# Optimization experiments

Hardware: AMD Instinct MI355X
Metric: run time of the kernel (lower is better)

## Reference

```python
import jax, jax.numpy as jnp
import numpy as np
from jax import lax

N, H, W, CIN = 64, 256, 256, 3   # batch, image HxW, RGB
C, K = 32, 5                     # cross-conv channels / kernel size (from reshape(-1,32,5,5))
ADIM, AHID = 4, 256              # action dim, action-encoder hidden


def _conv(x, w, b, stride, pad):
    # x [N,C,H,W], w [O,I,kh,kw] (torch OIHW cross-correlation semantics)
    y = lax.conv_general_dilated(x, w, (stride, stride), [(pad, pad), (pad, pad)],
                                 dimension_numbers=('NCHW', 'OIHW', 'NCHW'))
    return y + b[None, :, None, None]


def cross_convolve(feat, kernels):
    # feat [N,C,h,w], kernels [N,C,K,K]; per-sample per-channel 'same' conv (padding=2).
    # Equivalent to the original N*C loop of tiny F.conv2d calls: one depthwise
    # (grouped, feature_group_count=C) conv per sample, vmapped over the batch.
    def one(x, k):  # x [C,h,w], k [C,K,K]
        y = lax.conv_general_dilated(x[None], k[:, None], (1, 1), [(2, 2), (2, 2)],
                                     dimension_numbers=('NCHW', 'OIHW', 'NCHW'),
                                     feature_group_count=C)
        return y[0]
    return jax.vmap(one)(feat, kernels)


def setup_inputs() -> dict:
    key = jax.random.key(0)
    ks = jax.random.split(key, 10)
    g = lambda i, shape, s: jax.random.normal(ks[i], shape, jnp.float32) * s
    return {
        'images': jax.random.normal(ks[0], (N, H, W, CIN), jnp.float32),
        'actions': jax.random.normal(ks[1], (N, ADIM), jnp.float32),
        # phys_encoder: conv(3->32,k5,s2,p2) relu, conv(32->32,k5,s2,p2) relu
        'pe_w1': g(2, (C, CIN, 5, 5), 0.08), 'pe_b1': jnp.zeros((C,), jnp.float32),
        'pe_w2': g(3, (C, C, 5, 5), 0.04), 'pe_b2': jnp.zeros((C,), jnp.float32),
        # action_encoder MLP: ADIM -> AHID -> C*K*K (=800)
        'ae_w1': g(4, (ADIM, AHID), 0.3), 'ae_b1': jnp.zeros((AHID,), jnp.float32),
        'ae_w2': g(5, (AHID, C * K * K), 0.05), 'ae_b2': jnp.zeros((C * K * K,), jnp.float32),
        # motion_predictor: conv(32->32,k3,p1) relu, conv(32->2,k3,p1)
        'mp_w1': g(6, (C, C, 3, 3), 0.06), 'mp_b1': jnp.zeros((C,), jnp.float32),
        'mp_w2': g(7, (2, C, 3, 3), 0.06), 'mp_b2': jnp.zeros((2,), jnp.float32),
    }


def reference(images, actions, pe_w1, pe_b1, pe_w2, pe_b2,
              ae_w1, ae_b1, ae_w2, ae_b2, mp_w1, mp_b1, mp_w2, mp_b2):
    x = jnp.transpose(images, (0, 3, 1, 2))                 # NHWC -> NCHW
    h = jax.nn.relu(_conv(x, pe_w1, pe_b1, 2, 2))           # [N,32,128,128]
    h = jax.nn.relu(_conv(h, pe_w2, pe_b2, 2, 2))           # [N,32,64,64]
    a = jax.nn.relu(actions @ ae_w1 + ae_b1)
    a = (a @ ae_w2 + ae_b2).reshape(-1, C, K, K)            # per-sample kernels [N,32,5,5]
    sa = cross_convolve(h, a)                               # [N,32,64,64]
    f = jax.nn.relu(_conv(sa, mp_w1, mp_b1, 1, 1))
    flow = _conv(f, mp_w2, mp_b2, 1, 1)                     # [N,2,64,64]
    return flow
```

## Files before the change

### kernel.cpp

```cpp
#include <hip/hip_runtime.h>


typedef __attribute__((ext_vector_type(8))) short bf16x8;
typedef __attribute__((ext_vector_type(4))) float f32x4;
typedef __attribute__((ext_vector_type(16))) float f32x16;

__device__ __forceinline__ unsigned short f2bf(float f) {
    unsigned int u = __float_as_uint(f);
    u = (u + 0x7FFFu + ((u >> 16) & 1u)) >> 16;
    return (unsigned short)u;
}
__device__ __forceinline__ float bf2f(unsigned short h) {
    return __uint_as_float(((unsigned int)h) << 16);
}

__global__ __launch_bounds__(64) void zero_border2(unsigned int* t0, int R0, int p0,
                                                   unsigned int* t1, int R1, int p1) {
    unsigned int* t = blockIdx.y ? t1 : t0;
    const int R = blockIdx.y ? R1 : R0;
    const int pad = blockIdx.y ? p1 : p0;
    const int row = blockIdx.x % R;
    const int n = blockIdx.x / R;
    if (n >= 64) return;
    const int tid = threadIdx.x;
    unsigned int* rp = t + (size_t)(n * R + row) * R * 16;
    if (row < pad || row >= R - pad) {
        for (int i = tid; i < R * 16; i += 64) rp[i] = 0u;
    } else {
        for (int i = tid; i < pad * 16; i += 64) {
            rp[i] = 0u;
            rp[(size_t)(R - pad) * 16 + i] = 0u;
        }
    }
}

__global__ __launch_bounds__(64) void zero_border_eo(unsigned int* E, unsigned int* O) {
    unsigned int* t = blockIdx.y ? O : E;
    const int row = blockIdx.x % 132;
    const int n = blockIdx.x / 132;
    const int tid = threadIdx.x;
    unsigned int* rp = t + (size_t)(n * 132 + row) * (66 * 16);
    if (row < 2 || row >= 130) {
        for (int i = tid; i < 66 * 16; i += 64) rp[i] = 0u;
    } else if (tid < 16) {
        rp[tid] = 0u;
        rp[65 * 16 + tid] = 0u;
    }
}

__global__ __launch_bounds__(256) void pad_img_kernel(const float* __restrict__ img,
                                                      unsigned short* __restrict__ imgp) {
    const int py = blockIdx.x % 260;
    const int n  = blockIdx.x / 260;
    const int iy = py - 2;
    const bool rowok = (iy >= 0) && (iy < 256);
    const float* srow = img + ((size_t)n * 256 + (rowok ? iy : 0)) * 768;
    unsigned short* drow = imgp + (size_t)(n * 260 + py) * 1056;
    for (int s = threadIdx.x; s < 1056; s += 256) {
        int px = s >> 2, c = s & 3;
        int ix = px - 2;
        float v = 0.f;
        if (rowok && c < 3 && ix >= 0 && ix < 256) v = srow[ix * 3 + c];
        drow[s] = f2bf(v);
    }
}

__global__ __launch_bounds__(256) void repack_all(const float* __restrict__ pe_w1,
                                                  const float* __restrict__ pe_w2,
                                                  const float* __restrict__ mp_w1,
                                                  const float* __restrict__ mp_w2,
                                                  unsigned short* __restrict__ B1,
                                                  unsigned short* __restrict__ B2,
                                                  unsigned short* __restrict__ Bm1,
                                                  unsigned short* __restrict__ Bm2) {
    int idx = blockIdx.x * 256 + threadIdx.x;
    if (idx < 5120) {
        int kh = idx / 1024, r = idx % 1024, o = r / 32, k = r % 32, dx = k >> 2, c = k & 3;
        float v = (dx < 5 && c < 3) ? pe_w1[o * 75 + c * 25 + kh * 5 + dx] : 0.f;
        B1[idx] = f2bf(v);
    } else if (idx < 30720) {
        int i = idx - 5120;
        int co = i / 800, r = i % 800, ci = r / 25, tap = r % 25;
        B2[(tap * 32 + co) * 32 + ci] = f2bf(pe_w2[i]);
    } else if (idx < 39936) {
        int i = idx - 30720;
        int co = i / 288, r = i % 288, ci = r / 9, tap = r % 9;
        Bm1[(tap * 32 + co) * 32 + ci] = f2bf(mp_w1[i]);
    } else if (idx < 44544) {
        int i = idx - 39936;
        int tap = i / 512, r = i % 512, co = r / 32, ci = r % 32;
        float v = (co < 2) ? mp_w2[co * 288 + ci * 9 + tap] : 0.f;
        Bm2[i] = f2bf(v);
    }
}

__global__ __launch_bounds__(256) void mlp_kernel(const float* __restrict__ actions,
                                                  const float* __restrict__ w1,
                                                  const float* __restrict__ b1,
                                                  const float* __restrict__ w2,
                                                  const float* __restrict__ b2,
                                                  float* __restrict__ aout) {
    int n = blockIdx.y;
    int t = threadIdx.x;
    __shared__ float hid[256];
    float a0 = actions[n * 4 + 0], a1 = actions[n * 4 + 1];
    float a2 = actions[n * 4 + 2], a3 = actions[n * 4 + 3];
    float acc = b1[t];
    acc += a0 * w1[0 * 256 + t] + a1 * w1[1 * 256 + t] +
           a2 * w1[2 * 256 + t] + a3 * w1[3 * 256 + t];
    hid[t] = fmaxf(acc, 0.0f);
    __syncthreads();
    int o = blockIdx.x * 200 + t;
    if (t < 200) {
        float s = b2[o];
        #pragma unroll 4
        for (int i = 0; i < 256; ++i) s += hid[i] * w2[i * 800 + o];
        aout[n * 800 + o] = s;
    }
}

__global__ __launch_bounds__(256, 4) void conv1_mfma(const unsigned short* __restrict__ imgp,
                                                     const short* __restrict__ B1,
                                                     const float* __restrict__ bias,
                                                     unsigned short* __restrict__ h1e,
                                                     unsigned short* __restrict__ h1o) {
    const int tid = threadIdx.x;
    const int lane = tid & 63;
    const int w = tid >> 6;
    const int n = blockIdx.y;
    const int cohalf = w & 1;
    const int oy = blockIdx.x * 2 + (w >> 1);
    const int ml = lane & 15;
    const int kg = lane >> 4;

    bf16x8 bfrag[5];
    #pragma unroll
    for (int kh = 0; kh < 5; ++kh)
        bfrag[kh] = *(const bf16x8*)(B1 + ((kh * 32 + cohalf * 16 + ml) * 32 + kg * 8));
    const float bia = bias[cohalf * 16 + ml];
    const int co = cohalf * 16 + ml;

    f32x4 acc[8];
    #pragma unroll
    for (int t = 0; t < 8; ++t) acc[t] = (f32x4){bia, bia, bia, bia};

    #pragma unroll
    for (int kh = 0; kh < 5; ++kh) {
        const unsigned short* rowbase = imgp + (size_t)(n * 260 + 2 * oy + kh) * 1056;
        bf16x8 af[8];
        #pragma unroll
        for (int t = 0; t < 8; ++t) {
            const int px0 = 2 * (16 * t + ml) + 2 * kg;
            af[t] = *(const bf16x8*)(rowbase + px0 * 4);
        }
        __builtin_amdgcn_sched_barrier(0);
        #pragma unroll
        for (int t = 0; t < 8; ++t)
            acc[t] = __builtin_amdgcn_mfma_f32_16x16x32_bf16(af[t], bfrag[kh], acc[t], 0, 0, 0);
    }
    const size_t rowoff = ((size_t)(n * 132) + oy + 2) * 2112 + co;
    #pragma unroll
    for (int t = 0; t < 8; ++t) {
        #pragma unroll
        for (int r = 0; r < 4; ++r) {
            const int px = 16 * t + kg * 4 + r;
            const unsigned short v = f2bf(fmaxf(acc[t][r], 0.f));
            if ((r & 1) == 0) h1e[rowoff + (size_t)((px + 2) >> 1) * 32] = v;
            else              h1o[rowoff + (size_t)((px + 1) >> 1) * 32] = v;
        }
    }
}

__global__ __launch_bounds__(256, 4) void conv2_mfma32(const unsigned short* __restrict__ h1e,
                                                       const unsigned short* __restrict__ h1o,
                                                       const unsigned int* __restrict__ B,
                                                       const float* __restrict__ bias,
                                                       unsigned short* __restrict__ h2p) {
    __shared__ unsigned int Bs[5 * 32 * 20];
    const int tid = threadIdx.x;
    const int lane = tid & 63;
    const int w = tid >> 6;
    const int n = blockIdx.y;
    const int oy = blockIdx.x * 2 + (w >> 1);
    const int x0 = (w & 1) * 32;
    const int ml = lane & 31;
    const int kgrp = lane >> 5;

    const float bia = bias[ml];
    f32x16 accA, accB;
    #pragma unroll
    for (int r = 0; r < 16; ++r) { accA[r] = bia; accB[r] = 0.f; }

    const unsigned short* bbase = (const unsigned short*)Bs + ml * 40 + kgrp * 8;
    const int qbase = (x0 + ml) * 32 + kgrp * 8;

    for (int kh = 0; kh < 5; ++kh) {
        if (kh) __syncthreads();
        const unsigned int* src = B + kh * 2560;
        #pragma unroll
        for (int i = tid; i < 2560; i += 256) {
            int row = i >> 4, p = i & 15;
            Bs[row * 20 + p] = src[i];
        }
        __syncthreads();

        const size_t rowoff = ((size_t)(n * 132) + 2 * oy + kh) * 2112;
        const unsigned short* re = h1e + rowoff + qbase;
        const unsigned short* ro = h1o + rowoff + qbase;
        bf16x8 ae[6], ao[4];
        #pragma unroll
        for (int j = 0; j < 3; ++j) {
            ae[2 * j]     = *(const bf16x8*)(re + j * 32);
            ae[2 * j + 1] = *(const bf16x8*)(re + j * 32 + 16);
        }
        #pragma unroll
        for (int j = 0; j < 2; ++j) {
            ao[2 * j]     = *(const bf16x8*)(ro + j * 32);
            ao[2 * j + 1] = *(const bf16x8*)(ro + j * 32 + 16);
        }
        __builtin_amdgcn_sched_barrier(0);
        #pragma unroll
        for (int j = 0; j < 3; ++j) {
            const bf16x8 b0 = *(const bf16x8*)(bbase + (2 * j) * 1280);
            const bf16x8 b1 = *(const bf16x8*)(bbase + (2 * j) * 1280 + 16);
            accA = __builtin_amdgcn_mfma_f32_32x32x16_bf16(ae[2 * j], b0, accA, 0, 0, 0);
            accA = __builtin_amdgcn_mfma_f32_32x32x16_bf16(ae[2 * j + 1], b1, accA, 0, 0, 0);
        }
        #pragma unroll
        for (int j = 0; j < 2; ++j) {
            const bf16x8 b0 = *(const bf16x8*)(bbase + (2 * j + 1) * 1280);
            const bf16x8 b1 = *(const bf16x8*)(bbase + (2 * j + 1) * 1280 + 16);
            accB = __builtin_amdgcn_mfma_f32_32x32x16_bf16(ao[2 * j], b0, accB, 0, 0, 0);
            accB = __builtin_amdgcn_mfma_f32_32x32x16_bf16(ao[2 * j + 1], b1, accB, 0, 0, 0);
        }
    }
    #pragma unroll
    for (int r = 0; r < 16; ++r) {
        const int px = (r & 3) + 8 * (r >> 2) + 4 * kgrp;
        const int ox = x0 + px;
        h2p[((size_t)(n * 68 + oy + 2) * 68 + ox + 2) * 32 + ml] =
            f2bf(fmaxf(accA[r] + accB[r], 0.f));
    }
}

__global__ __launch_bounds__(256) void xconv_kernel(const unsigned short* __restrict__ h2p,
                                                    const float* __restrict__ ker,
                                                    unsigned short* __restrict__ sap) {
    __shared__ __align__(16) unsigned short tile[12 * 68 * 32];
    const int tid = threadIdx.x;
    const int n = blockIdx.x;
    const int rb = blockIdx.y;
    const unsigned short* src = h2p + (size_t)(n * 68 + rb * 8) * (68 * 32);
    for (int i = tid; i < 3264; i += 256)
        *(uint4*)(tile + i * 8) = *(const uint4*)(src + i * 8);
    const int ci = tid & 31, xg = tid >> 5;
    const float* kp = ker + (size_t)(n * 32 + ci) * 25;
    float k[25];
    #pragma unroll
    for (int t = 0; t < 25; ++t) k[t] = kp[t];
    __syncthreads();

    float acc[8][8];
    #pragma unroll
    for (int r = 0; r < 8; ++r)
        #pragma unroll
        for (int j = 0; j < 8; ++j) acc[r][j] = 0.f;

    #pragma unroll
    for (int ir = 0; ir < 12; ++ir) {
        float v[12];
        #pragma unroll
        for (int t = 0; t < 12; ++t)
            v[t] = bf2f(tile[(ir * 68 + xg * 8 + t) * 32 + ci]);
        #pragma unroll
        for (int kh = 0; kh < 5; ++kh) {
            const int r = ir - kh;
            if (r >= 0 && r < 8) {
                #pragma unroll
                for (int j = 0; j < 8; ++j) {
                    float s = acc[r][j];
                    #pragma unroll
                    for (int kw = 0; kw < 5; ++kw) s += k[kh * 5 + kw] * v[j + kw];
                    acc[r][j] = s;
                }
            }
        }
    }
    #pragma unroll
    for (int r = 0; r < 8; ++r)
        #pragma unroll
        for (int j = 0; j < 8; ++j)
            sap[((size_t)(n * 66 + rb * 8 + r + 1) * 66 + xg * 8 + j + 1) * 32 + ci] = f2bf(acc[r][j]);
}

__global__ __launch_bounds__(256, 4) void mp1_mfma32(const unsigned short* __restrict__ sap,
                                                     const unsigned int* __restrict__ B,
                                                     const float* __restrict__ bias,
                                                     unsigned short* __restrict__ fp) {
    __shared__ unsigned int Bs[9 * 32 * 20];
    const int tid = threadIdx.x;
    #pragma unroll
    for (int i = tid; i < 4608; i += 256) {
        int row = i >> 4, p = i & 15;
        Bs[row * 20 + p] = B[i];
    }
    __syncthreads();

    const int lane = tid & 63;
    const int w = tid >> 6;
    const int n = blockIdx.y;
    const int oy = blockIdx.x * 2 + (w >> 1);
    const int x0 = (w & 1) * 32;
    const int ml = lane & 31;
    const int kgrp = lane >> 5;

    const float bia = bias[ml];
    f32x16 accA, accB;
    #pragma unroll
    for (int r = 0; r < 16; ++r) { accA[r] = bia; accB[r] = 0.f; }

    const unsigned short* bbase = (const unsigned short*)Bs + ml * 40 + kgrp * 8;
    const int px0 = x0 + ml;

    #pragma unroll
    for (int kh = 0; kh < 3; ++kh) {
        const unsigned short* rowbase = sap + (size_t)(n * 66 + oy + kh) * 2112 + kgrp * 8;
        bf16x8 a[6];
        #pragma unroll
        for (int kw = 0; kw < 3; ++kw) {
            a[2 * kw]     = *(const bf16x8*)(rowbase + (px0 + kw) * 32);
            a[2 * kw + 1] = *(const bf16x8*)(rowbase + (px0 + kw) * 32 + 16);
        }
        __builtin_amdgcn_sched_barrier(0);
        #pragma unroll
        for (int kw = 0; kw < 3; ++kw) {
            const int tap = kh * 3 + kw;
            const bf16x8 b0 = *(const bf16x8*)(bbase + tap * 1280);
            const bf16x8 b1 = *(const bf16x8*)(bbase + tap * 1280 + 16);
            if (tap & 1) {
                accB = __builtin_amdgcn_mfma_f32_32x32x16_bf16(a[2 * kw], b0, accB, 0, 0, 0);
                accB = __builtin_amdgcn_mfma_f32_32x32x16_bf16(a[2 * kw + 1], b1, accB, 0, 0, 0);
            } else {
                accA = __builtin_amdgcn_mfma_f32_32x32x16_bf16(a[2 * kw], b0, accA, 0, 0, 0);
                accA = __builtin_amdgcn_mfma_f32_32x32x16_bf16(a[2 * kw + 1], b1, accA, 0, 0, 0);
            }
        }
    }
    #pragma unroll
    for (int r = 0; r < 16; ++r) {
        const int px = (r & 3) + 8 * (r >> 2) + 4 * kgrp;
        const int ox = x0 + px;
        fp[((size_t)(n * 66 + oy + 1) * 66 + ox + 1) * 32 + ml] =
            f2bf(fmaxf(accA[r] + accB[r], 0.f));
    }
}

__global__ __launch_bounds__(256, 4) void mp2_mfma(const unsigned short* __restrict__ fpb,
                                                   const short* __restrict__ B,
                                                   const float* __restrict__ bias,
                                                   float* __restrict__ out) {
    const int tid = threadIdx.x;
    const int lane = tid & 63;
    const int w = tid >> 6;
    const int n = blockIdx.y;
    const int oy = blockIdx.x * 4 + w;
    const int ml = lane & 15;
    const int kg = lane >> 4;

    bf16x8 bfrag[9];
    #pragma unroll
    for (int t = 0; t < 9; ++t)
        bfrag[t] = *(const bf16x8*)(B + ((t * 16 + ml) * 32 + kg * 8));
    const float bia = (ml < 2) ? bias[ml] : 0.f;

    f32x4 acc[4];
    #pragma unroll
    for (int t = 0; t < 4; ++t) acc[t] = (f32x4){bia, bia, bia, bia};

    #pragma unroll
    for (int kh = 0; kh < 3; ++kh) {
        const unsigned short* rowbase = fpb + (size_t)(n * 66 + oy + kh) * (66 * 32);
        bf16x8 af[12];
        #pragma unroll
        for (int kw = 0; kw < 3; ++kw)
            #pragma unroll
            for (int t = 0; t < 4; ++t)
                af[kw * 4 + t] = *(const bf16x8*)(rowbase + (16 * t + ml + kw) * 32 + kg * 8);
        __builtin_amdgcn_sched_barrier(0);
        #pragma unroll
        for (int kw = 0; kw < 3; ++kw)
            #pragma unroll
            for (int t = 0; t < 4; ++t)
                acc[t] = __builtin_amdgcn_mfma_f32_16x16x32_bf16(af[kw * 4 + t], bfrag[kh * 3 + kw], acc[t], 0, 0, 0);
    }
    if (ml < 2) {
        #pragma unroll
        for (int t = 0; t < 4; ++t) {
            #pragma unroll
            for (int r = 0; r < 4; ++r) {
                const int px = 16 * t + kg * 4 + r;
                out[(size_t)n * 8192 + (size_t)ml * 4096 + (size_t)oy * 64 + px] = acc[t][r];
            }
        }
    }
}

extern "C" void kernel_launch(void* const* d_in, const int* in_sizes, int n_in,
                              void* d_out, int out_size, void* d_ws, size_t ws_size,
                              hipStream_t stream) {
    (void)in_sizes; (void)n_in; (void)out_size; (void)ws_size;
    const float* images  = (const float*)d_in[0];
    const float* actions = (const float*)d_in[1];
    const float* pe_w1   = (const float*)d_in[2];
    const float* pe_b1   = (const float*)d_in[3];
    const float* pe_w2   = (const float*)d_in[4];
    const float* pe_b2   = (const float*)d_in[5];
    const float* ae_w1   = (const float*)d_in[6];
    const float* ae_b1   = (const float*)d_in[7];
    const float* ae_w2   = (const float*)d_in[8];
    const float* ae_b2   = (const float*)d_in[9];
    const float* mp_w1   = (const float*)d_in[10];
    const float* mp_b1   = (const float*)d_in[11];
    const float* mp_w2   = (const float*)d_in[12];
    const float* mp_b2   = (const float*)d_in[13];
    float* out = (float*)d_out;

    char* ws = (char*)d_ws;
    float* a_ker          = (float*)(ws + 0);
    unsigned short* B1    = (unsigned short*)(ws + 204800);
    unsigned short* B2    = (unsigned short*)(ws + 215040);
    unsigned short* Bm1   = (unsigned short*)(ws + 266240);
    unsigned short* Bm2   = (unsigned short*)(ws + 284672);
    unsigned short* h1e   = (unsigned short*)(ws + 524288);
    unsigned short* h1o   = (unsigned short*)(ws + 36208640);
    unsigned short* imgp  = (unsigned short*)(ws + 71892992);
    unsigned short* h2p   = (unsigned short*)(ws + 71892992);
    unsigned short* sap   = (unsigned short*)(ws + 90832896);
    unsigned short* fpb   = (unsigned short*)(ws + 108675072);

    repack_all<<<174, 256, 0, stream>>>(pe_w1, pe_w2, mp_w1, mp_w2, B1, B2, Bm1, Bm2);
    mlp_kernel<<<dim3(4, 64), 256, 0, stream>>>(actions, ae_w1, ae_b1, ae_w2, ae_b2, a_ker);
    zero_border_eo<<<dim3(64 * 132, 2), 64, 0, stream>>>((unsigned int*)h1e, (unsigned int*)h1o);
    zero_border2<<<dim3(64 * 66, 1), 64, 0, stream>>>((unsigned int*)fpb, 66, 1,
                                                      (unsigned int*)fpb, 66, 1);

    pad_img_kernel<<<64 * 260, 256, 0, stream>>>(images, imgp);
    conv1_mfma<<<dim3(64, 64), 256, 0, stream>>>(imgp, (const short*)B1, pe_b1, h1e, h1o);

    zero_border2<<<dim3(64 * 68, 2), 64, 0, stream>>>((unsigned int*)h2p, 68, 2,
                                                      (unsigned int*)sap, 66, 1);

    conv2_mfma32<<<dim3(32, 64), 256, 0, stream>>>(h1e, h1o, (const unsigned int*)B2, pe_b2, h2p);
    xconv_kernel<<<dim3(64, 8), 256, 0, stream>>>(h2p, a_ker, sap);
    mp1_mfma32<<<dim3(32, 64), 256, 0, stream>>>(sap, (const unsigned int*)Bm1, mp_b1, fpb);
    mp2_mfma<<<dim3(16, 64), 256, 0, stream>>>(fpb, (const short*)Bm2, mp_b2, out);
}
```

Baseline: 279.5 us.

## Swap MFMA operands to vectorize channel-contiguous epilogue stores across conv kernels

Conv1, conv2 and mp1 now pass the weight fragment as the MFMA A operand, so each lane's accumulator rows cover consecutive output channels. That lets the epilogues pack four bf16 values into a single 8-byte store instead of issuing scattered 2-byte stores. Bias is added at the end from a vector load rather than used to seed the accumulators. The cross-conv kernel stages its output through shared memory so it can write 16-byte coalesced rows, and the image pad kernel now writes one packed 8-byte pixel per thread. In exchange this adds extra shared-memory traffic and syncs in the cross-conv kernel.

```diff
diff --git a/kernel.cpp b/kernel.cpp
--- a/kernel.cpp
+++ b/kernel.cpp
@@ -9,6 +9,9 @@
     unsigned int u = __float_as_uint(f);
     u = (u + 0x7FFFu + ((u >> 16) & 1u)) >> 16;
     return (unsigned short)u;
+}
+__device__ __forceinline__ unsigned int pk2(float lo, float hi) {
+    return (unsigned int)f2bf(lo) | ((unsigned int)f2bf(hi) << 16);
 }
 __device__ __forceinline__ float bf2f(unsigned short h) {
     return __uint_as_float(((unsigned int)h) << 16);
@@ -56,12 +59,14 @@
     const bool rowok = (iy >= 0) && (iy < 256);
     const float* srow = img + ((size_t)n * 256 + (rowok ? iy : 0)) * 768;
     unsigned short* drow = imgp + (size_t)(n * 260 + py) * 1056;
-    for (int s = threadIdx.x; s < 1056; s += 256) {
-        int px = s >> 2, c = s & 3;
-        int ix = px - 2;
-        float v = 0.f;
-        if (rowok && c < 3 && ix >= 0 && ix < 256) v = srow[ix * 3 + c];
-        drow[s] = f2bf(v);
+    for (int px = threadIdx.x; px < 264; px += 256) {
+        const int ix = px - 2;
+        float c0 = 0.f, c1 = 0.f, c2 = 0.f;
+        if (rowok && ix >= 0 && ix < 256) {
+            c0 = srow[ix * 3 + 0]; c1 = srow[ix * 3 + 1]; c2 = srow[ix * 3 + 2];
+        }
+        uint2 u; u.x = pk2(c0, c1); u.y = pk2(c2, 0.f);
+        *(uint2*)(drow + px * 4) = u;
     }
 }
 
@@ -137,12 +142,10 @@
     #pragma unroll
     for (int kh = 0; kh < 5; ++kh)
         bfrag[kh] = *(const bf16x8*)(B1 + ((kh * 32 + cohalf * 16 + ml) * 32 + kg * 8));
-    const float bia = bias[cohalf * 16 + ml];
-    const int co = cohalf * 16 + ml;
 
     f32x4 acc[8];
     #pragma unroll
-    for (int t = 0; t < 8; ++t) acc[t] = (f32x4){bia, bia, bia, bia};
+    for (int t = 0; t < 8; ++t) acc[t] = (f32x4){0.f, 0.f, 0.f, 0.f};
 
     #pragma unroll
     for (int kh = 0; kh < 5; ++kh) {
@@ -156,18 +159,19 @@
         __builtin_amdgcn_sched_barrier(0);
         #pragma unroll
         for (int t = 0; t < 8; ++t)
-            acc[t] = __builtin_amdgcn_mfma_f32_16x16x32_bf16(af[t], bfrag[kh], acc[t], 0, 0, 0);
-    }
-    const size_t rowoff = ((size_t)(n * 132) + oy + 2) * 2112 + co;
+            acc[t] = __builtin_amdgcn_mfma_f32_16x16x32_bf16(bfrag[kh], af[t], acc[t], 0, 0, 0);
+    }
+    const f32x4 b4 = *(const f32x4*)(bias + cohalf * 16 + kg * 4);
+    const int cobase = cohalf * 16 + kg * 4;
+    const size_t rowoff = ((size_t)(n * 132) + oy + 2) * 2112;
     #pragma unroll
     for (int t = 0; t < 8; ++t) {
-        #pragma unroll
-        for (int r = 0; r < 4; ++r) {
-            const int px = 16 * t + kg * 4 + r;
-            const unsigned short v = f2bf(fmaxf(acc[t][r], 0.f));
-            if ((r & 1) == 0) h1e[rowoff + (size_t)((px + 2) >> 1) * 32] = v;
-            else              h1o[rowoff + (size_t)((px + 1) >> 1) * 32] = v;
-        }
+        const int px = 16 * t + ml;
+        uint2 uv;
+        uv.x = pk2(fmaxf(acc[t][0] + b4[0], 0.f), fmaxf(acc[t][1] + b4[1], 0.f));
+        uv.y = pk2(fmaxf(acc[t][2] + b4[2], 0.f), fmaxf(acc[t][3] + b4[3], 0.f));
+        if (ml & 1) *(uint2*)(h1o + rowoff + (size_t)((px + 1) >> 1) * 32 + cobase) = uv;
+        else        *(uint2*)(h1e + rowoff + (size_t)((px + 2) >> 1) * 32 + cobase) = uv;
     }
 }
 
@@ -186,10 +190,9 @@
     const int ml = lane & 31;
     const int kgrp = lane >> 5;
 
-    const float bia = bias[ml];
     f32x16 accA, accB;
     #pragma unroll
-    for (int r = 0; r < 16; ++r) { accA[r] = bia; accB[r] = 0.f; }
+    for (int r = 0; r < 16; ++r) { accA[r] = 0.f; accB[r] = 0.f; }
 
     const unsigned short* bbase = (const unsigned short*)Bs + ml * 40 + kgrp * 8;
     const int qbase = (x0 + ml) * 32 + kgrp * 8;
@@ -223,23 +226,30 @@
         for (int j = 0; j < 3; ++j) {
             const bf16x8 b0 = *(const bf16x8*)(bbase + (2 * j) * 1280);
             const bf16x8 b1 = *(const bf16x8*)(bbase + (2 * j) * 1280 + 16);
-            accA = __builtin_amdgcn_mfma_f32_32x32x16_bf16(ae[2 * j], b0, accA, 0, 0, 0);
-            accA = __builtin_amdgcn_mfma_f32_32x32x16_bf16(ae[2 * j + 1], b1, accA, 0, 0, 0);
+            accA = __builtin_amdgcn_mfma_f32_32x32x16_bf16(b0, ae[2 * j], accA, 0, 0, 0);
+            accA = __builtin_amdgcn_mfma_f32_32x32x16_bf16(b1, ae[2 * j + 1], accA, 0, 0, 0);
         }
         #pragma unroll
         for (int j = 0; j < 2; ++j) {
             const bf16x8 b0 = *(const bf16x8*)(bbase + (2 * j + 1) * 1280);
             const bf16x8 b1 = *(const bf16x8*)(bbase + (2 * j + 1) * 1280 + 16);
-            accB = __builtin_amdgcn_mfma_f32_32x32x16_bf16(ao[2 * j], b0, accB, 0, 0, 0);
-            accB = __builtin_amdgcn_mfma_f32_32x32x16_bf16(ao[2 * j + 1], b1, accB, 0, 0, 0);
-        }
-    }
-    #pragma unroll
-    for (int r = 0; r < 16; ++r) {
-        const int px = (r & 3) + 8 * (r >> 2) + 4 * kgrp;
-        const int ox = x0 + px;
-        h2p[((size_t)(n * 68 + oy + 2) * 68 + ox + 2) * 32 + ml] =
-            f2bf(fmaxf(accA[r] + accB[r], 0.f));
+            accB = __builtin_amdgcn_mfma_f32_32x32x16_bf16(b0, ao[2 * j], accB, 0, 0, 0);
+            accB = __builtin_amdgcn_mfma_f32_32x32x16_bf16(b1, ao[2 * j + 1], accB, 0, 0, 0);
+        }
+    }
+    const int px = x0 + ml;
+    unsigned short* dst = h2p + ((size_t)(n * 68 + oy + 2) * 68 + px + 2) * 32;
+    #pragma unroll
+    for (int g = 0; g < 4; ++g) {
+        const f32x4 b4 = *(const f32x4*)(bias + 8 * g + 4 * kgrp);
+        float a0 = accA[4 * g + 0] + accB[4 * g + 0] + b4[0];
+        float a1 = accA[4 * g + 1] + accB[4 * g + 1] + b4[1];
+        float a2 = accA[4 * g + 2] + accB[4 * g + 2] + b4[2];
+        float a3 = accA[4 * g + 3] + accB[4 * g + 3] + b4[3];
+        uint2 uv;
+        uv.x = pk2(fmaxf(a0, 0.f), fmaxf(a1, 0.f));
+        uv.y = pk2(fmaxf(a2, 0.f), fmaxf(a3, 0.f));
+        *(uint2*)(dst + 8 * g + 4 * kgrp) = uv;
     }
 }
 
@@ -286,11 +296,18 @@
             }
         }
     }
+    __syncthreads();
     #pragma unroll
     for (int r = 0; r < 8; ++r)
         #pragma unroll
         for (int j = 0; j < 8; ++j)
-            sap[((size_t)(n * 66 + rb * 8 + r + 1) * 66 + xg * 8 + j + 1) * 32 + ci] = f2bf(acc[r][j]);
+            tile[(r * 64 + xg * 8 + j) * 32 + ci] = f2bf(acc[r][j]);
+    __syncthreads();
+    #pragma unroll
+    for (int r = 0; r < 8; ++r) {
+        uint4 v = *(const uint4*)(tile + (size_t)r * 2048 + tid * 8);
+        *(uint4*)(sap + ((size_t)(n * 66 + rb * 8 + r + 1) * 66 + 1) * 32 + tid * 8) = v;
+    }
 }
 
 __global__ __launch_bounds__(256, 4) void mp1_mfma32(const unsigned short* __restrict__ sap,
@@ -314,10 +331,9 @@
     const int ml = lane & 31;
     const int kgrp = lane >> 5;
 
-    const float bia = bias[ml];
     f32x16 accA, accB;
     #pragma unroll
-    for (int r = 0; r < 16; ++r) { accA[r] = bia; accB[r] = 0.f; }
+    for (int r = 0; r < 16; ++r) { accA[r] = 0.f; accB[r] = 0.f; }
 
     const unsigned short* bbase = (const unsigned short*)Bs + ml * 40 + kgrp * 8;
     const int px0 = x0 + ml;
@@ -338,20 +354,27 @@
             const bf16x8 b0 = *(const bf16x8*)(bbase + tap * 1280);
             const bf16x8 b1 = *(const bf16x8*)(bbase + tap * 1280 + 16);
             if (tap & 1) {
-                accB = __builtin_amdgcn_mfma_f32_32x32x16_bf16(a[2 * kw], b0, accB, 0, 0, 0);
-                accB = __builtin_amdgcn_mfma_f32_32x32x16_bf16(a[2 * kw + 1], b1, accB, 0, 0, 0);
+                accB = __builtin_amdgcn_mfma_f32_32x32x16_bf16(b0, a[2 * kw], accB, 0, 0, 0);
+                accB = __builtin_amdgcn_mfma_f32_32x32x16_bf16(b1, a[2 * kw + 1], accB, 0, 0, 0);
             } else {
-                accA = __builtin_amdgcn_mfma_f32_32x32x16_bf16(a[2 * kw], b0, accA, 0, 0, 0);
-                accA = __builtin_amdgcn_mfma_f32_32x32x16_bf16(a[2 * kw + 1], b1, accA, 0, 0, 0);
+                accA = __builtin_amdgcn_mfma_f32_32x32x16_bf16(b0, a[2 * kw], accA, 0, 0, 0);
+                accA = __builtin_amdgcn_mfma_f32_32x32x16_bf16(b1, a[2 * kw + 1], accA, 0, 0, 0);
             }
         }
     }
-    #pragma unroll
-    for (int r = 0; r < 16; ++r) {
-        const int px = (r & 3) + 8 * (r >> 2) + 4 * kgrp;
-        const int ox = x0 + px;
-        fp[((size_t)(n * 66 + oy + 1) * 66 + ox + 1) * 32 + ml] =
-            f2bf(fmaxf(accA[r] + accB[r], 0.f));
+    const int px = x0 + ml;
+    unsigned short* dst = fp + ((size_t)(n * 66 + oy + 1) * 66 + px + 1) * 32;
+    #pragma unroll
+    for (int g = 0; g < 4; ++g) {
+        const f32x4 b4 = *(const f32x4*)(bias + 8 * g + 4 * kgrp);
+        float a0 = accA[4 * g + 0] + accB[4 * g + 0] + b4[0];
+        float a1 = accA[4 * g + 1] + accB[4 * g + 1] + b4[1];
+        float a2 = accA[4 * g + 2] + accB[4 * g + 2] + b4[2];
+        float a3 = accA[4 * g + 3] + accB[4 * g + 3] + b4[3];
+        uint2 uv;
+        uv.x = pk2(fmaxf(a0, 0.f), fmaxf(a1, 0.f));
+        uv.y = pk2(fmaxf(a2, 0.f), fmaxf(a3, 0.f));
+        *(uint2*)(dst + 8 * g + 4 * kgrp) = uv;
     }
 }
 
```

Result: no change. 277.0 us (-0.9%).
